# Performance work log

Measured on AMD Instinct MI355X. Metric: run time of the kernel, lower is better.

## Reference

```python
import jax, jax.numpy as jnp
import numpy as np

D_MODEL = 512
D_STATE = 16
D_CONV = 3
EXPAND = 2
D_INNER = EXPAND * D_MODEL          # 1024
DT_RANK = -(-D_MODEL // 16)          # ceil(d_model/16) = 32
BATCH = 2
SEQ = 1024


def setup_inputs() -> dict:
    key = jax.random.key(0)
    ks = jax.random.split(key, 8)
    s = 0.02
    x = jax.random.normal(ks[0], (BATCH, SEQ, D_MODEL), jnp.float32)
    in_proj_w = jax.random.normal(ks[1], (2 * D_INNER, D_MODEL), jnp.float32) * s
    conv_w = jax.random.normal(ks[2], (D_INNER, 1, D_CONV), jnp.float32) * 0.2  # depthwise (out, in/groups=1, K)
    conv_b = jnp.zeros((D_INNER,), jnp.float32)
    x_proj_w = jax.random.normal(ks[3], (DT_RANK + 4 * D_STATE + 1, D_INNER), jnp.float32) * s
    dt_std = DT_RANK ** -0.5
    dt_w = jax.random.uniform(ks[4], (D_INNER, DT_RANK), jnp.float32, -dt_std, dt_std)
    dt = jnp.exp(jax.random.uniform(ks[5], (D_INNER,), jnp.float32)
                 * (np.log(0.1) - np.log(0.001)) + np.log(0.001))
    dt = jnp.maximum(dt, 1e-4)
    dt_b = dt + jnp.log(-jnp.expm1(-dt))  # inverse-softplus init, as in torch code
    A_log = jnp.log(jnp.tile(jnp.arange(1, D_STATE + 1, dtype=jnp.float32)[None, :], (D_INNER, 1)))
    A_imag = np.pi * jax.random.uniform(ks[6], (D_INNER, D_STATE), jnp.float32)
    D_skip = jnp.ones((D_INNER,), jnp.float32)
    out_proj_w = jax.random.normal(ks[7], (D_MODEL, D_INNER), jnp.float32) * s
    return {"x": x, "in_proj_w": in_proj_w, "conv_w": conv_w, "conv_b": conv_b,
            "x_proj_w": x_proj_w, "dt_w": dt_w, "dt_b": dt_b,
            "A_log": A_log, "A_imag": A_imag, "D_skip": D_skip,
            "out_proj_w": out_proj_w}


def _combine(c1, c2):
    # linear recurrence h_t = a_t * h_{t-1} + u_t as an associative op
    a1, u1 = c1
    a2, u2 = c2
    return a1 * a2, a2 * u1 + u2


def reference(x, in_proj_w, conv_w, conv_b, x_proj_w, dt_w, dt_b,
              A_log, A_imag, D_skip, out_proj_w):
    Bsz, L, _ = x.shape
    d_state = A_log.shape[1]
    dt_rank = dt_w.shape[1]

    xz = x @ in_proj_w.T                     # (B, L, 2*D_inner)
    xi, z = jnp.split(xz, 2, axis=-1)

    # causal depthwise conv1d (torch pads both sides K-1 then slices [:L] == left-pad K-1)
    xc = jax.lax.conv_general_dilated(
        xi.transpose(0, 2, 1), conv_w, window_strides=(1,),
        padding=[(D_CONV - 1, 0)], dimension_numbers=("NCH", "OIH", "NCH"),
        feature_group_count=conv_w.shape[0])
    xc = (xc + conv_b[None, :, None]).transpose(0, 2, 1)   # (B, L, D_inner)
    xc = jax.nn.silu(xc)

    A = -jnp.exp(A_log) + 1j * A_imag         # (D_inner, N) complex64

    proj = xc @ x_proj_w.T                     # (B, L, dt_rank + 4N + 1)
    splits = np.cumsum([dt_rank, d_state, d_state, d_state, d_state])
    delta_raw, B_re, B_im, C_re, C_im, lam = jnp.split(proj, splits, axis=-1)
    delta = jax.nn.softplus(delta_raw @ dt_w.T + dt_b)     # (B, L, D_inner)
    lam = jax.nn.sigmoid(lam)                              # (B, L, 1)
    Bc = B_re + 1j * B_im                                  # (B, L, N)
    Cc = C_re + 1j * C_im                                  # (B, L, N)

    # selective_scan_v3 (trapezoidal discretization)
    alpha = jnp.exp(delta[..., None] * A[None, None])      # (B, L, D, N) complex
    Bx = Bc[:, :, None, :] * xc[..., None]                 # (B, L, D, N) complex
    beta = (1.0 - lam)[..., None] * delta[..., None] * alpha
    gamma = lam[..., None] * delta[..., None]
    Bx_prev = jnp.pad(Bx[:, :-1], ((0, 0), (1, 0), (0, 0), (0, 0)))
    u = beta * Bx_prev + gamma * Bx                        # (B, L, D, N) complex

    _, hs = jax.lax.associative_scan(_combine, (alpha, u), axis=1)

    y = jnp.real(jnp.sum(hs * jnp.conj(Cc)[:, :, None, :], axis=-1))  # (B, L, D)
    y = y + D_skip * xc
    out = (y * jax.nn.silu(z)) @ out_proj_w.T              # (B, L, d_model)
    return out
```

## Files before the change

kernel.cpp:

```cpp
#include <hip/hip_runtime.h>

constexpr int B  = 2, L = 1024, DM = 512, DI = 1024, NST = 16, PW = 97;
constexpr int ML = B * L;
constexpr int NCHUNK = 32, CL = L / NCHUNK;
constexpr int NLANES = B * DI * NST;

#define DEV_INLINE __device__ __forceinline__

typedef __attribute__((ext_vector_type(8))) short bf16x8;
typedef __attribute__((ext_vector_type(4))) float f32x4;

DEV_INLINE float sigmoidf_(float x) { return 1.f / (1.f + __expf(-x)); }
DEV_INLINE unsigned short f2bf(float f) {
  unsigned int u = __float_as_uint(f);
  return (unsigned short)((u + 0x7FFFu + ((u >> 16) & 1u)) >> 16);
}

#if __has_builtin(__builtin_amdgcn_exp2f)
#define EXP2F(x) __builtin_amdgcn_exp2f(x)
#else
#define EXP2F(x) exp2f(x)
#endif
#if __has_builtin(__builtin_amdgcn_sinf)
#define SINR(x) __builtin_amdgcn_sinf(x)
#define COSR(x) __builtin_amdgcn_cosf(x)
#else
#define SINR(x) __sinf((x) * 6.2831853f)
#define COSR(x) __cosf((x) * 6.2831853f)
#endif

DEV_INLINE void sincos_poly(float th, float& s, float& c) {
  float t2 = th * th;
  float u = fmaf(t2, -1.9841270e-4f, 8.3333333e-3f);
  u = fmaf(t2, u, -0.16666667f);
  u = fmaf(t2, u, 1.f);
  s = th * u;
  float v = fmaf(t2, -1.3888889e-3f, 4.1666667e-2f);
  v = fmaf(t2, v, -0.5f);
  c = fmaf(t2, v, 1.f);
}

template <int CTRL>
DEV_INLINE float dpp_add(float v) {
  int x = __builtin_amdgcn_update_dpp(0, __float_as_int(v), CTRL, 0xF, 0xF, true);
  return v + __int_as_float(x);
}

__global__ __launch_bounds__(256) void cvt3_k(
    const float* __restrict__ i0, unsigned short* __restrict__ o0, int n0,
    const float* __restrict__ i1, unsigned short* __restrict__ o1, int n1,
    const float* __restrict__ i2, unsigned short* __restrict__ o2, int n2) {
  int i = blockIdx.x * 256 + threadIdx.x;
  const float* in; unsigned short* out; int off;
  if (i < n0)              { in = i0; out = o0; off = i; }
  else if (i < n0 + n1)    { in = i1; out = o1; off = i - n0; }
  else if (i < n0 + n1 + n2) { in = i2; out = o2; off = i - n0 - n1; }
  else return;
  float4 v = ((const float4*)in)[off];
  ((ushort4*)out)[off] = make_ushort4(f2bf(v.x), f2bf(v.y), f2bf(v.z), f2bf(v.w));
}

DEV_INLINE int swz(int row, int kb) { return (row << 7) + (kb ^ ((row & 7) << 4)); }

__global__ __launch_bounds__(256) void gemm_bf16_64(
    const short* __restrict__ A, const short* __restrict__ W,
    float* __restrict__ C, int M, int N, int K) {
  __shared__ char ldsb[16384];
  const int tid = threadIdx.x;
  const int lane = tid & 63, wv = tid >> 6;
  const int bm = blockIdx.y * 64, bn = blockIdx.x * 64;

  f32x4 acc[4];
#pragma unroll
  for (int nb = 0; nb < 4; ++nb) acc[nb] = (f32x4){0.f, 0.f, 0.f, 0.f};

  for (int k0 = 0; k0 < K; k0 += 64) {
#pragma unroll
    for (int i = 0; i < 2; ++i) {
      int off = i * 4096 + tid * 16;
      int row = off >> 7, kb = off & 127;
      bf16x8 va = *(const bf16x8*)(A + (size_t)(bm + row) * K + k0 + (kb >> 1));
      bf16x8 vw = *(const bf16x8*)(W + (size_t)(bn + row) * K + k0 + (kb >> 1));
      *(bf16x8*)(ldsb + swz(row, kb)) = va;
      *(bf16x8*)(ldsb + 8192 + swz(row, kb)) = vw;
    }
    __syncthreads();
#pragma unroll
    for (int ks = 0; ks < 2; ++ks) {
      const int kb = ks * 64 + ((lane >> 4) << 4);
      bf16x8 af = *(const bf16x8*)(ldsb + swz(wv * 16 + (lane & 15), kb));
#pragma unroll
      for (int nb = 0; nb < 4; ++nb) {
        bf16x8 bfv = *(const bf16x8*)(ldsb + 8192 + swz(nb * 16 + (lane & 15), kb));
        acc[nb] = __builtin_amdgcn_mfma_f32_16x16x32_bf16(af, bfv, acc[nb], 0, 0, 0);
      }
    }
    __syncthreads();
  }
#pragma unroll
  for (int nb = 0; nb < 4; ++nb) {
    int col = bn + nb * 16 + (lane & 15);
    int row0 = bm + wv * 16 + ((lane >> 4) << 2);
#pragma unroll
    for (int j = 0; j < 4; ++j)
      C[(size_t)(row0 + j) * N + col] = acc[nb][j];
  }
}

__global__ __launch_bounds__(256) void gemm_bf16_64_sk(
    const short* __restrict__ A, const short* __restrict__ W,
    float* __restrict__ P, int M, int N, int K) {
  __shared__ char ldsb[16384];
  const int tid = threadIdx.x;
  const int lane = tid & 63, wv = tid >> 6;
  const int bm = blockIdx.y * 64, bn = blockIdx.x * 64;
  const int kz = blockIdx.z * 256;
  float* Cp = P + (size_t)blockIdx.z * M * N;

  f32x4 acc[4];
#pragma unroll
  for (int nb = 0; nb < 4; ++nb) acc[nb] = (f32x4){0.f, 0.f, 0.f, 0.f};

  for (int k0 = kz; k0 < kz + 256; k0 += 64) {
#pragma unroll
    for (int i = 0; i < 2; ++i) {
      int off = i * 4096 + tid * 16;
      int row = off >> 7, kb = off & 127;
      bf16x8 va = *(const bf16x8*)(A + (size_t)(bm + row) * K + k0 + (kb >> 1));
      bf16x8 vw = *(const bf16x8*)(W + (size_t)(bn + row) * K + k0 + (kb >> 1));
      *(bf16x8*)(ldsb + swz(row, kb)) = va;
      *(bf16x8*)(ldsb + 8192 + swz(row, kb)) = vw;
    }
    __syncthreads();
#pragma unroll
    for (int ks = 0; ks < 2; ++ks) {
      const int kb = ks * 64 + ((lane >> 4) << 4);
      bf16x8 af = *(const bf16x8*)(ldsb + swz(wv * 16 + (lane & 15), kb));
#pragma unroll
      for (int nb = 0; nb < 4; ++nb) {
        bf16x8 bfv = *(const bf16x8*)(ldsb + 8192 + swz(nb * 16 + (lane & 15), kb));
        acc[nb] = __builtin_amdgcn_mfma_f32_16x16x32_bf16(af, bfv, acc[nb], 0, 0, 0);
      }
    }
    __syncthreads();
  }
#pragma unroll
  for (int nb = 0; nb < 4; ++nb) {
    int col = bn + nb * 16 + (lane & 15);
    int row0 = bm + wv * 16 + ((lane >> 4) << 2);
#pragma unroll
    for (int j = 0; j < 4; ++j)
      Cp[(size_t)(row0 + j) * N + col] = acc[nb][j];
  }
}

__global__ __launch_bounds__(256) void addp4_k(
    const float4* __restrict__ p, float4* __restrict__ out) {
  constexpr int NN = ML * DM / 4;
  int i = blockIdx.x * 256 + threadIdx.x;
  float4 a = p[i], b = p[i + NN], c = p[i + 2 * NN], d = p[i + 3 * NN];
  out[i] = make_float4(a.x + b.x + c.x + d.x, a.y + b.y + c.y + d.y,
                       a.z + b.z + c.z + d.z, a.w + b.w + c.w + d.w);
}

__global__ __launch_bounds__(256) void conv_silu_k(
    const float* __restrict__ xz, const float* __restrict__ cw,
    const float* __restrict__ cb, float* __restrict__ xc, float* __restrict__ sz) {
  int idx = blockIdx.x * 256 + threadIdx.x;
  int m = idx >> 8, d4 = (idx & 255) * 4;
  int t = m & (L - 1);
  const float* base = xz + (size_t)m * (2 * DI);
  float4 r2 = *(const float4*)(base + d4);
  float4 r1 = (t >= 1) ? *(const float4*)(base - 2 * DI + d4) : make_float4(0, 0, 0, 0);
  float4 r0 = (t >= 2) ? *(const float4*)(base - 4 * DI + d4) : make_float4(0, 0, 0, 0);
  float4 zv = *(const float4*)(base + DI + d4);
  float wv[12];
  *(float4*)(wv + 0) = *(const float4*)(cw + d4 * 3 + 0);
  *(float4*)(wv + 4) = *(const float4*)(cw + d4 * 3 + 4);
  *(float4*)(wv + 8) = *(const float4*)(cw + d4 * 3 + 8);
  float4 bv = *(const float4*)(cb + d4);
  float rin0[4] = {r0.x, r0.y, r0.z, r0.w};
  float rin1[4] = {r1.x, r1.y, r1.z, r1.w};
  float rin2[4] = {r2.x, r2.y, r2.z, r2.w};
  float bb[4] = {bv.x, bv.y, bv.z, bv.w};
  float zz[4] = {zv.x, zv.y, zv.z, zv.w};
  float xo[4], zo[4];
#pragma unroll
  for (int j = 0; j < 4; ++j) {
    float v = bb[j];
    v = fmaf(rin0[j], wv[3 * j + 0], v);
    v = fmaf(rin1[j], wv[3 * j + 1], v);
    v = fmaf(rin2[j], wv[3 * j + 2], v);
    xo[j] = v * sigmoidf_(v);
    zo[j] = zz[j] * sigmoidf_(zz[j]);
  }
  *(float4*)(xc + (size_t)idx * 4) = make_float4(xo[0], xo[1], xo[2], xo[3]);
  *(float4*)(sz + (size_t)idx * 4) = make_float4(zo[0], zo[1], zo[2], zo[3]);
}

__global__ __launch_bounds__(512) void proj_delta_k(
    const float* __restrict__ xc, const float* __restrict__ xw,
    const float* __restrict__ dtw, const float* __restrict__ dtb,
    float* __restrict__ bc2f, float* __restrict__ cc2f,
    float* __restrict__ lamv, float2* __restrict__ dx2) {
  __shared__ float xs[4][DI];
  __shared__ float pt[3][4][128];
  __shared__ float dts[4][32];
  const int tid = threadIdx.x;
  const int m0 = blockIdx.x * 4;
  const int nn = tid & 127, qq = tid >> 7;
  for (int i = tid; i < 4 * DI; i += 512)
    xs[i >> 10][i & 1023] = xc[(size_t)m0 * DI + i];
  __syncthreads();
  float s0 = 0.f, s1 = 0.f, s2 = 0.f, s3 = 0.f;
  if (nn < PW) {
    const float* wr = xw + (size_t)nn * DI + qq * 256;
    const int kb = qq * 256;
#pragma unroll 4
    for (int k = 0; k < 256; k += 4) {
      float4 w4 = *(const float4*)(wr + k);
      s0 = fmaf(xs[0][kb + k], w4.x, s0); s0 = fmaf(xs[0][kb + k + 1], w4.y, s0);
      s0 = fmaf(xs[0][kb + k + 2], w4.z, s0); s0 = fmaf(xs[0][kb + k + 3], w4.w, s0);
      s1 = fmaf(xs[1][kb + k], w4.x, s1); s1 = fmaf(xs[1][kb + k + 1], w4.y, s1);
      s1 = fmaf(xs[1][kb + k + 2], w4.z, s1); s1 = fmaf(xs[1][kb + k + 3], w4.w, s1);
      s2 = fmaf(xs[2][kb + k], w4.x, s2); s2 = fmaf(xs[2][kb + k + 1], w4.y, s2);
      s2 = fmaf(xs[2][kb + k + 2], w4.z, s2); s2 = fmaf(xs[2][kb + k + 3], w4.w, s2);
      s3 = fmaf(xs[3][kb + k], w4.x, s3); s3 = fmaf(xs[3][kb + k + 1], w4.y, s3);
      s3 = fmaf(xs[3][kb + k + 2], w4.z, s3); s3 = fmaf(xs[3][kb + k + 3], w4.w, s3);
    }
    if (qq > 0) {
      pt[qq - 1][0][nn] = s0; pt[qq - 1][1][nn] = s1;
      pt[qq - 1][2][nn] = s2; pt[qq - 1][3][nn] = s3;
    }
  }
  __syncthreads();
  if (qq == 0 && nn < PW) {
    s0 += pt[0][0][nn] + pt[1][0][nn] + pt[2][0][nn];
    s1 += pt[0][1][nn] + pt[1][1][nn] + pt[2][1][nn];
    s2 += pt[0][2][nn] + pt[1][2][nn] + pt[2][2][nn];
    s3 += pt[0][3][nn] + pt[1][3][nn] + pt[2][3][nn];
    float sv[4] = {s0, s1, s2, s3};
#pragma unroll
    for (int r = 0; r < 4; ++r) {
      int m = m0 + r;
      float s = sv[r];
      if (nn < 32)        dts[r][nn] = s;
      else if (nn < 48)   bc2f[(m * 16 + nn - 32) * 2 + 0] = s;
      else if (nn < 64)   bc2f[(m * 16 + nn - 48) * 2 + 1] = s;
      else if (nn < 80)   cc2f[(m * 16 + nn - 64) * 2 + 0] = s;
      else if (nn < 96)   cc2f[(m * 16 + nn - 80) * 2 + 1] = s;
      else                lamv[m] = sigmoidf_(s);
    }
  }
  __syncthreads();
  {
    const int d = tid * 2;
    const float4* dtw4 = (const float4*)dtw;
    float2 bb = *(const float2*)(dtb + d);
    float a0[4], a1[4];
#pragma unroll
    for (int r = 0; r < 4; ++r) { a0[r] = bb.x; a1[r] = bb.y; }
#pragma unroll
    for (int kq = 0; kq < 8; ++kq) {
      float4 wa = dtw4[d * 8 + kq];
      float4 wb = dtw4[(d + 1) * 8 + kq];
#pragma unroll
      for (int r = 0; r < 4; ++r) {
        a0[r] = fmaf(dts[r][kq * 4 + 0], wa.x, a0[r]);
        a0[r] = fmaf(dts[r][kq * 4 + 1], wa.y, a0[r]);
        a0[r] = fmaf(dts[r][kq * 4 + 2], wa.z, a0[r]);
        a0[r] = fmaf(dts[r][kq * 4 + 3], wa.w, a0[r]);
        a1[r] = fmaf(dts[r][kq * 4 + 0], wb.x, a1[r]);
        a1[r] = fmaf(dts[r][kq * 4 + 1], wb.y, a1[r]);
        a1[r] = fmaf(dts[r][kq * 4 + 2], wb.z, a1[r]);
        a1[r] = fmaf(dts[r][kq * 4 + 3], wb.w, a1[r]);
      }
    }
#pragma unroll
    for (int r = 0; r < 4; ++r) {
      float x0 = a0[r], x1 = a1[r];
      float dl0 = (x0 > 20.f) ? x0 : log1pf(__expf(x0));
      float dl1 = (x1 > 20.f) ? x1 : log1pf(__expf(x1));
      float4 o = make_float4(dl0, xs[r][d], dl1, xs[r][d + 1]);
      *(float4*)(dx2 + (size_t)(m0 + r) * DI + d) = o;
    }
  }
}

template <bool PASS_B>
__global__ __launch_bounds__(256, 8) void scan_pass(
    const float2* __restrict__ dx2, const float* __restrict__ lamv,
    const float2* __restrict__ bc2, const float2* __restrict__ cc2,
    const float* __restrict__ sz,
    const float* __restrict__ A_log, const float* __restrict__ A_imag,
    const float* __restrict__ D_skip,
    float2* __restrict__ aggA, float2* __restrict__ aggU,
    unsigned short* __restrict__ ybuf) {
  __shared__ float4 qx[CL][17];
  __shared__ float2 bcl[CL][17];
  __shared__ float2 ccl[PASS_B ? CL : 1][17];
  __shared__ float  ylds[PASS_B ? CL : 1][17];

  const int tid = threadIdx.x;
  const int n = tid & 15, ch = tid >> 4;
  const int bx = blockIdx.x, c = blockIdx.y;
  const int b = bx >> 6, d0 = (bx & 63) * 16;
  const int d = d0 + ch;
  const int lane = bx * 256 + tid;
  const int t0 = c * CL, mb = b * L;

  {
    int t = tid >> 3, pr = tid & 7;
    size_t row = (size_t)(mb + t0 + t);
    float4 v = *(const float4*)(dx2 + row * DI + d0 + pr * 2);
    float lamt = lamv[row];
    float g0 = lamt * v.x, g1 = lamt * v.z;
    qx[t][pr * 2 + 0] = make_float4(v.x, v.y, v.x - g0, g0);
    qx[t][pr * 2 + 1] = make_float4(v.z, v.w, v.z - g1, g1);
    float4 bv = *(const float4*)(bc2 + row * 16 + pr * 2);
    bcl[t][pr * 2 + 0] = make_float2(bv.x, bv.y);
    bcl[t][pr * 2 + 1] = make_float2(bv.z, bv.w);
    if constexpr (PASS_B) {
      float4 cv = *(const float4*)(cc2 + row * 16 + pr * 2);
      ccl[t][pr * 2 + 0] = make_float2(cv.x, cv.y);
      ccl[t][pr * 2 + 1] = make_float2(cv.z, cv.w);
    }
  }

  const float Ar = -__expf(A_log[d * 16 + n]);
  const float Arl = Ar * 1.44269504f;
  const float Ai = A_imag[d * 16 + n];

  float Bxpr = 0.f, Bxpi = 0.f;
  if (c > 0) {
    float xp = dx2[(size_t)(mb + t0 - 1) * DI + d].y;
    float2 bp = bc2[(size_t)(mb + t0 - 1) * 16 + n];
    Bxpr = bp.x * xp; Bxpi = bp.y * xp;
  }
  float hr = 0.f, hi = 0.f, S = 0.f, Dsk = 0.f;
  if (PASS_B) {
    if (c > 0) {
      float2 h0 = aggU[(c - 1) * NLANES + lane];
      hr = h0.x; hi = h0.y;
    }
    Dsk = D_skip[d];
  }

  __syncthreads();

#pragma unroll
  for (int t = 0; t < CL; ++t) {
    float4 q = qx[t][ch];
    float2 bv = bcl[t][n];
    float ear = EXP2F(q.x * Arl);
    float sn, cs; sincos_poly(q.x * Ai, sn, cs);
    float ar = ear * cs, ai = ear * sn;
    float Bxr = bv.x * q.y, Bxi = bv.y * q.y;
    float wr = fmaf(q.z, Bxpr, hr), wi = fmaf(q.z, Bxpi, hi);
    hr = fmaf(q.w, Bxr, fmaf(-ai, wi, ar * wr));
    hi = fmaf(q.w, Bxi, fmaf(ai, wr, ar * wi));
    Bxpr = Bxr; Bxpi = Bxi;
    if constexpr (!PASS_B) {
      S += q.x;
    } else {
      float2 cv = ccl[t][n];
      float yc = fmaf(hi, cv.y, hr * cv.x);
      yc = dpp_add<0xB1>(yc);
      yc = dpp_add<0x4E>(yc);
      yc = dpp_add<0x124>(yc);
      yc = dpp_add<0x128>(yc);
      if (n == 0) ylds[t][ch] = fmaf(Dsk, q.y, yc);
    }
  }

  if constexpr (!PASS_B) {
    float earS = EXP2F(S * Arl);
    float rvS = S * Ai * 0.15915494f;
    float AaR = earS * COSR(rvS);
    float AaI = earS * SINR(rvS);
    int idx = c * NLANES + lane;
    aggA[idx] = make_float2(AaR, AaI);
    aggU[idx] = make_float2(hr, hi);
  } else {
    __syncthreads();
    int t = tid >> 3, pr = tid & 7;
    size_t row = (size_t)(mb + t0 + t);
    float2 szv = *(const float2*)(sz + row * DI + d0 + pr * 2);
    float y0 = ylds[t][pr * 2 + 0] * szv.x;
    float y1 = ylds[t][pr * 2 + 1] * szv.y;
    unsigned pk = (unsigned)f2bf(y0) | ((unsigned)f2bf(y1) << 16);
    *(unsigned*)(ybuf + row * DI + d0 + pr * 2) = pk;
  }
}

__global__ __launch_bounds__(256) void scan_combine_k(
    const float2* __restrict__ aggA, float2* __restrict__ aggU) {
  int gid = blockIdx.x * 256 + threadIdx.x;
  float hr = 0.f, hi = 0.f;
#pragma unroll
  for (int c = 0; c < NCHUNK - 1; ++c) {
    float2 a = aggA[c * NLANES + gid];
    float2 u = aggU[c * NLANES + gid];
    float nr = fmaf(a.x, hr, fmaf(-a.y, hi, u.x));
    float ni = fmaf(a.x, hi, fmaf(a.y, hr, u.y));
    hr = nr; hi = ni;
    aggU[c * NLANES + gid] = make_float2(hr, hi);
  }
}

extern "C" void kernel_launch(void* const* d_in, const int* in_sizes, int n_in,
                              void* d_out, int out_size, void* d_ws, size_t ws_size,
                              hipStream_t stream) {
  const float* x        = (const float*)d_in[0];
  const float* in_proj  = (const float*)d_in[1];
  const float* conv_w   = (const float*)d_in[2];
  const float* conv_b   = (const float*)d_in[3];
  const float* x_proj_w = (const float*)d_in[4];
  const float* dt_w     = (const float*)d_in[5];
  const float* dt_b     = (const float*)d_in[6];
  const float* A_log    = (const float*)d_in[7];
  const float* A_imag   = (const float*)d_in[8];
  const float* D_skip   = (const float*)d_in[9];
  const float* out_proj = (const float*)d_in[10];
  float* out = (float*)d_out;

  float* ws = (float*)d_ws;
  float*  xz    = ws; ws += (size_t)ML * 2 * DI;
  float*  xc    = ws; ws += (size_t)ML * DI;
  float*  sz    = ws; ws += (size_t)ML * DI;
  float2* dx2   = (float2*)ws; ws += (size_t)ML * DI * 2;
  float*  bc2f  = ws; ws += (size_t)ML * 32;
  float*  cc2f  = ws; ws += (size_t)ML * 32;
  float*  lamv  = ws; ws += ML;
  float2* aggA  = (float2*)ws; ws += (size_t)NCHUNK * NLANES * 2;
  float2* aggU  = (float2*)ws; ws += (size_t)NCHUNK * NLANES * 2;
  unsigned short* xb   = (unsigned short*)ws; ws += (size_t)ML * DM / 2;
  unsigned short* wb1  = (unsigned short*)ws; ws += (size_t)(2 * DI) * DM / 2;
  unsigned short* wb2  = (unsigned short*)ws; ws += (size_t)DM * DI / 2;
  unsigned short* ybuf = (unsigned short*)ws; ws += (size_t)ML * DI / 2;

  const int n0 = ML * DM / 4, n1 = 2 * DI * DM / 4, n2 = DM * DI / 4;
  cvt3_k<<<(n0 + n1 + n2 + 255) / 256, 256, 0, stream>>>(x, xb, n0, in_proj, wb1, n1,
                                                         out_proj, wb2, n2);
  gemm_bf16_64<<<dim3(2 * DI / 64, ML / 64), 256, 0, stream>>>(
      (const short*)xb, (const short*)wb1, xz, ML, 2 * DI, DM);
  conv_silu_k<<<ML * DI / 4 / 256, 256, 0, stream>>>(xz, conv_w, conv_b, xc, sz);
  proj_delta_k<<<ML / 4, 512, 0, stream>>>(xc, x_proj_w, dt_w, dt_b,
                                           bc2f, cc2f, lamv, dx2);
  scan_pass<false><<<dim3(128, NCHUNK - 1), 256, 0, stream>>>(
      dx2, lamv, (const float2*)bc2f, (const float2*)cc2f, sz,
      A_log, A_imag, D_skip, aggA, aggU, nullptr);
  scan_combine_k<<<NLANES / 256, 256, 0, stream>>>(aggA, aggU);
  scan_pass<true><<<dim3(128, NCHUNK), 256, 0, stream>>>(
      dx2, lamv, (const float2*)bc2f, (const float2*)cc2f, sz,
      A_log, A_imag, D_skip, aggA, aggU, ybuf);
  gemm_bf16_64_sk<<<dim3(DM / 64, ML / 64, 4), 256, 0, stream>>>(
      (const short*)ybuf, (const short*)wb2, xz, ML, DM, DI);
  addp4_k<<<ML * DM / 4 / 256, 256, 0, stream>>>((const float4*)xz, (float4*)out);
}
```

Before: 141.2 us.

## Split x_proj into tiled split-K FP32 GEMM plus reduce and delta kernels

```diff
diff --git a/kernel.cpp b/kernel.cpp
--- a/kernel.cpp
+++ b/kernel.cpp
@@ -60,6 +60,14 @@
   ((ushort4*)out)[off] = make_ushort4(f2bf(v.x), f2bf(v.y), f2bf(v.z), f2bf(v.w));
 }
 
+__global__ __launch_bounds__(256) void padw_k(
+    const float* __restrict__ xw, float* __restrict__ xwp) {
+  int i = blockIdx.x * 256 + threadIdx.x;
+  int row = i >> 8;
+  float4 v = (row < PW) ? ((const float4*)xw)[i] : make_float4(0, 0, 0, 0);
+  ((float4*)xwp)[i] = v;
+}
+
 DEV_INLINE int swz(int row, int kb) { return (row << 7) + (kb ^ ((row & 7) << 4)); }
 
 __global__ __launch_bounds__(256) void gemm_bf16_64(
@@ -161,6 +169,63 @@
   float4 a = p[i], b = p[i + NN], c = p[i + 2 * NN], d = p[i + 3 * NN];
   out[i] = make_float4(a.x + b.x + c.x + d.x, a.y + b.y + c.y + d.y,
                        a.z + b.z + c.z + d.z, a.w + b.w + c.w + d.w);
+}
+
+__global__ __launch_bounds__(256) void proj_sk_f32(
+    const float* __restrict__ A, const float* __restrict__ W,
+    float* __restrict__ P) {
+  __shared__ float As[16][68];
+  __shared__ float Ws[16][68];
+  const int tid = threadIdx.x;
+  const int tx = tid & 15, ty = tid >> 4;
+  const int bm = blockIdx.y * 64, bn = blockIdx.x * 64;
+  const int kz = blockIdx.z * 128;
+  float acc[4][4] = {};
+  for (int k0 = kz; k0 < kz + 128; k0 += 16) {
+    const int r = tid >> 2, c4 = (tid & 3) * 4;
+    float4 av = *(const float4*)(A + (size_t)(bm + r) * DI + k0 + c4);
+    float4 wv = *(const float4*)(W + (size_t)(bn + r) * DI + k0 + c4);
+    As[c4 + 0][r] = av.x; As[c4 + 1][r] = av.y; As[c4 + 2][r] = av.z; As[c4 + 3][r] = av.w;
+    Ws[c4 + 0][r] = wv.x; Ws[c4 + 1][r] = wv.y; Ws[c4 + 2][r] = wv.z; Ws[c4 + 3][r] = wv.w;
+    __syncthreads();
+#pragma unroll
+    for (int kk = 0; kk < 16; ++kk) {
+      float a[4], b[4];
+#pragma unroll
+      for (int i = 0; i < 4; ++i) a[i] = As[kk][ty * 4 + i];
+#pragma unroll
+      for (int j = 0; j < 4; ++j) b[j] = Ws[kk][tx * 4 + j];
+#pragma unroll
+      for (int i = 0; i < 4; ++i)
+#pragma unroll
+        for (int j = 0; j < 4; ++j) acc[i][j] = fmaf(a[i], b[j], acc[i][j]);
+    }
+    __syncthreads();
+  }
+  float* Cp = P + (size_t)blockIdx.z * ML * 128;
+#pragma unroll
+  for (int i = 0; i < 4; ++i) {
+    float4 v = make_float4(acc[i][0], acc[i][1], acc[i][2], acc[i][3]);
+    *(float4*)(Cp + (size_t)(bm + ty * 4 + i) * 128 + bn + tx * 4) = v;
+  }
+}
+
+__global__ __launch_bounds__(256) void reduce_pack_k(
+    const float* __restrict__ P, float* __restrict__ dtp,
+    float* __restrict__ bc2f, float* __restrict__ cc2f,
+    float* __restrict__ lamv) {
+  int i = blockIdx.x * 256 + threadIdx.x;
+  int m = i >> 7, c = i & 127;
+  if (c >= PW) return;
+  float s = 0.f;
+#pragma unroll
+  for (int z = 0; z < 8; ++z) s += P[(size_t)z * ML * 128 + i];
+  if (c < 32)       dtp[m * 32 + c] = s;
+  else if (c < 48)  bc2f[(m * 16 + c - 32) * 2 + 0] = s;
+  else if (c < 64)  bc2f[(m * 16 + c - 48) * 2 + 1] = s;
+  else if (c < 80)  cc2f[(m * 16 + c - 64) * 2 + 0] = s;
+  else if (c < 96)  cc2f[(m * 16 + c - 80) * 2 + 1] = s;
+  else              lamv[m] = sigmoidf_(s);
 }
 
 __global__ __launch_bounds__(256) void conv_silu_k(
@@ -198,92 +263,42 @@
   *(float4*)(sz + (size_t)idx * 4) = make_float4(zo[0], zo[1], zo[2], zo[3]);
 }
 
-__global__ __launch_bounds__(512) void proj_delta_k(
-    const float* __restrict__ xc, const float* __restrict__ xw,
-    const float* __restrict__ dtw, const float* __restrict__ dtb,
-    float* __restrict__ bc2f, float* __restrict__ cc2f,
-    float* __restrict__ lamv, float2* __restrict__ dx2) {
-  __shared__ float xs[4][DI];
-  __shared__ float pt[3][4][128];
-  __shared__ float dts[4][32];
+__global__ __launch_bounds__(256) void delta_k(
+    const float* __restrict__ dtp, const float* __restrict__ dtw,
+    const float* __restrict__ dtb, const float* __restrict__ xc,
+    float2* __restrict__ dx2) {
+  __shared__ float ws[256][33];
+  __shared__ float ps[8][32];
   const int tid = threadIdx.x;
-  const int m0 = blockIdx.x * 4;
-  const int nn = tid & 127, qq = tid >> 7;
-  for (int i = tid; i < 4 * DI; i += 512)
-    xs[i >> 10][i & 1023] = xc[(size_t)m0 * DI + i];
+  const int d0 = blockIdx.x * 256;
+  const int m0 = blockIdx.y * 8;
+#pragma unroll
+  for (int j = 0; j < 8; ++j) {
+    int flat = tid * 4 + j * 1024;
+    int r = flat >> 5, c = flat & 31;
+    float4 v = *(const float4*)(dtw + (size_t)d0 * 32 + flat);
+    ws[r][c] = v.x; ws[r][c + 1] = v.y; ws[r][c + 2] = v.z; ws[r][c + 3] = v.w;
+  }
+  { int i = tid >> 5, r = tid & 31;
+    ps[i][r] = dtp[(size_t)(m0 + i) * 32 + r]; }
   __syncthreads();
-  float s0 = 0.f, s1 = 0.f, s2 = 0.f, s3 = 0.f;
-  if (nn < PW) {
-    const float* wr = xw + (size_t)nn * DI + qq * 256;
-    const int kb = qq * 256;
-#pragma unroll 4
-    for (int k = 0; k < 256; k += 4) {
-      float4 w4 = *(const float4*)(wr + k);
-      s0 = fmaf(xs[0][kb + k], w4.x, s0); s0 = fmaf(xs[0][kb + k + 1], w4.y, s0);
-      s0 = fmaf(xs[0][kb + k + 2], w4.z, s0); s0 = fmaf(xs[0][kb + k + 3], w4.w, s0);
-      s1 = fmaf(xs[1][kb + k], w4.x, s1); s1 = fmaf(xs[1][kb + k + 1], w4.y, s1);
-      s1 = fmaf(xs[1][kb + k + 2], w4.z, s1); s1 = fmaf(xs[1][kb + k + 3], w4.w, s1);
-      s2 = fmaf(xs[2][kb + k], w4.x, s2); s2 = fmaf(xs[2][kb + k + 1], w4.y, s2);
-      s2 = fmaf(xs[2][kb + k + 2], w4.z, s2); s2 = fmaf(xs[2][kb + k + 3], w4.w, s2);
-      s3 = fmaf(xs[3][kb + k], w4.x, s3); s3 = fmaf(xs[3][kb + k + 1], w4.y, s3);
-      s3 = fmaf(xs[3][kb + k + 2], w4.z, s3); s3 = fmaf(xs[3][kb + k + 3], w4.w, s3);
-    }
-    if (qq > 0) {
-      pt[qq - 1][0][nn] = s0; pt[qq - 1][1][nn] = s1;
-      pt[qq - 1][2][nn] = s2; pt[qq - 1][3][nn] = s3;
-    }
-  }
-  __syncthreads();
-  if (qq == 0 && nn < PW) {
-    s0 += pt[0][0][nn] + pt[1][0][nn] + pt[2][0][nn];
-    s1 += pt[0][1][nn] + pt[1][1][nn] + pt[2][1][nn];
-    s2 += pt[0][2][nn] + pt[1][2][nn] + pt[2][2][nn];
-    s3 += pt[0][3][nn] + pt[1][3][nn] + pt[2][3][nn];
-    float sv[4] = {s0, s1, s2, s3};
-#pragma unroll
-    for (int r = 0; r < 4; ++r) {
-      int m = m0 + r;
-      float s = sv[r];
-      if (nn < 32)        dts[r][nn] = s;
-      else if (nn < 48)   bc2f[(m * 16 + nn - 32) * 2 + 0] = s;
-      else if (nn < 64)   bc2f[(m * 16 + nn - 48) * 2 + 1] = s;
-      else if (nn < 80)   cc2f[(m * 16 + nn - 64) * 2 + 0] = s;
-      else if (nn < 96)   cc2f[(m * 16 + nn - 80) * 2 + 1] = s;
-      else                lamv[m] = sigmoidf_(s);
-    }
-  }
-  __syncthreads();
-  {
-    const int d = tid * 2;
-    const float4* dtw4 = (const float4*)dtw;
-    float2 bb = *(const float2*)(dtb + d);
-    float a0[4], a1[4];
-#pragma unroll
-    for (int r = 0; r < 4; ++r) { a0[r] = bb.x; a1[r] = bb.y; }
-#pragma unroll
-    for (int kq = 0; kq < 8; ++kq) {
-      float4 wa = dtw4[d * 8 + kq];
-      float4 wb = dtw4[(d + 1) * 8 + kq];
-#pragma unroll
-      for (int r = 0; r < 4; ++r) {
-        a0[r] = fmaf(dts[r][kq * 4 + 0], wa.x, a0[r]);
-        a0[r] = fmaf(dts[r][kq * 4 + 1], wa.y, a0[r]);
-        a0[r] = fmaf(dts[r][kq * 4 + 2], wa.z, a0[r]);
-        a0[r] = fmaf(dts[r][kq * 4 + 3], wa.w, a0[r]);
-        a1[r] = fmaf(dts[r][kq * 4 + 0], wb.x, a1[r]);
-        a1[r] = fmaf(dts[r][kq * 4 + 1], wb.y, a1[r]);
-        a1[r] = fmaf(dts[r][kq * 4 + 2], wb.z, a1[r]);
-        a1[r] = fmaf(dts[r][kq * 4 + 3], wb.w, a1[r]);
-      }
-    }
-#pragma unroll
-    for (int r = 0; r < 4; ++r) {
-      float x0 = a0[r], x1 = a1[r];
-      float dl0 = (x0 > 20.f) ? x0 : log1pf(__expf(x0));
-      float dl1 = (x1 > 20.f) ? x1 : log1pf(__expf(x1));
-      float4 o = make_float4(dl0, xs[r][d], dl1, xs[r][d + 1]);
-      *(float4*)(dx2 + (size_t)(m0 + r) * DI + d) = o;
-    }
+  float s[8];
+  float bias = dtb[d0 + tid];
+#pragma unroll
+  for (int i = 0; i < 8; ++i) s[i] = bias;
+#pragma unroll
+  for (int r = 0; r < 32; ++r) {
+    float wv = ws[tid][r];
+#pragma unroll
+    for (int i = 0; i < 8; ++i) s[i] = fmaf(ps[i][r], wv, s[i]);
+  }
+#pragma unroll
+  for (int i = 0; i < 8; ++i) {
+    float x = s[i];
+    float dlt = (x > 20.f) ? x : log1pf(__expf(x));
+    int m = m0 + i;
+    float xt = xc[(size_t)m * DI + d0 + tid];
+    dx2[(size_t)m * DI + d0 + tid] = make_float2(dlt, xt);
   }
 }
 
@@ -429,9 +444,11 @@
   float*  xc    = ws; ws += (size_t)ML * DI;
   float*  sz    = ws; ws += (size_t)ML * DI;
   float2* dx2   = (float2*)ws; ws += (size_t)ML * DI * 2;
+  float*  dtp   = ws; ws += (size_t)ML * 32;
   float*  bc2f  = ws; ws += (size_t)ML * 32;
   float*  cc2f  = ws; ws += (size_t)ML * 32;
   float*  lamv  = ws; ws += ML;
+  float*  xwp   = ws; ws += (size_t)128 * DI;
   float2* aggA  = (float2*)ws; ws += (size_t)NCHUNK * NLANES * 2;
   float2* aggU  = (float2*)ws; ws += (size_t)NCHUNK * NLANES * 2;
   unsigned short* xb   = (unsigned short*)ws; ws += (size_t)ML * DM / 2;
@@ -442,11 +459,13 @@
   const int n0 = ML * DM / 4, n1 = 2 * DI * DM / 4, n2 = DM * DI / 4;
   cvt3_k<<<(n0 + n1 + n2 + 255) / 256, 256, 0, stream>>>(x, xb, n0, in_proj, wb1, n1,
                                                          out_proj, wb2, n2);
+  padw_k<<<128, 256, 0, stream>>>(x_proj_w, xwp);
   gemm_bf16_64<<<dim3(2 * DI / 64, ML / 64), 256, 0, stream>>>(
       (const short*)xb, (const short*)wb1, xz, ML, 2 * DI, DM);
   conv_silu_k<<<ML * DI / 4 / 256, 256, 0, stream>>>(xz, conv_w, conv_b, xc, sz);
-  proj_delta_k<<<ML / 4, 512, 0, stream>>>(xc, x_proj_w, dt_w, dt_b,
-                                           bc2f, cc2f, lamv, dx2);
+  proj_sk_f32<<<dim3(2, ML / 64, 8), 256, 0, stream>>>(xc, xwp, xz);
+  reduce_pack_k<<<ML * 128 / 256, 256, 0, stream>>>(xz, dtp, bc2f, cc2f, lamv);
+  delta_k<<<dim3(DI / 256, ML / 8), 256, 0, stream>>>(dtp, dt_w, dt_b, xc, dx2);
   scan_pass<false><<<dim3(128, NCHUNK - 1), 256, 0, stream>>>(
       dx2, lamv, (const float2*)bc2f, (const float2*)cc2f, sz,
       A_log, A_imag, D_skip, aggA, aggU, nullptr);
```

New measurement: 141.2 us. Within noise of the previous version (+0.0%).

## Move x_proj onto bf16 MFMA split-K GEMM and stage tiles with global_load_lds

Applied to the files above, without the earlier changes.

```diff
diff --git a/kernel.cpp b/kernel.cpp
--- a/kernel.cpp
+++ b/kernel.cpp
@@ -29,6 +29,16 @@
 #define COSR(x) __cosf((x) * 6.2831853f)
 #endif
 
+#if __has_builtin(__builtin_amdgcn_global_load_lds)
+#define HAVE_GLDS 1
+#define GLOAD16(g, l)                                                         \
+  __builtin_amdgcn_global_load_lds(                                           \
+      (const __attribute__((address_space(1))) unsigned int*)(g),             \
+      (__attribute__((address_space(3))) unsigned int*)(l), 16, 0, 0)
+#else
+#define HAVE_GLDS 0
+#endif
+
 DEV_INLINE void sincos_poly(float th, float& s, float& c) {
   float t2 = th * th;
   float u = fmaf(t2, -1.9841270e-4f, 8.3333333e-3f);
@@ -60,7 +70,45 @@
   ((ushort4*)out)[off] = make_ushort4(f2bf(v.x), f2bf(v.y), f2bf(v.z), f2bf(v.w));
 }
 
+__global__ __launch_bounds__(256) void padw_bf16_k(
+    const float* __restrict__ xw, unsigned short* __restrict__ xwpb) {
+  int i = blockIdx.x * 256 + threadIdx.x;
+  int row = i >> 8;
+  float4 v = (row < PW) ? ((const float4*)xw)[i] : make_float4(0, 0, 0, 0);
+  ((ushort4*)xwpb)[i] = make_ushort4(f2bf(v.x), f2bf(v.y), f2bf(v.z), f2bf(v.w));
+}
+
 DEV_INLINE int swz(int row, int kb) { return (row << 7) + (kb ^ ((row & 7) << 4)); }
+
+#define GEMM_STAGE(Abase, Wbase)                                              \
+  _Pragma("unroll")                                                           \
+  for (int i = 0; i < 2; ++i) {                                               \
+    int off = i * 4096 + tid * 16;                                            \
+    int row = off >> 7, kb = off & 127;                                       \
+    int kel = (kb ^ ((row & 7) << 4)) >> 1;                                   \
+    stage16(Abase + (size_t)(bm + row) * K + k0 + kel, ldsb + off);           \
+    stage16(Wbase + (size_t)(bn + row) * K + k0 + kel, ldsb + 8192 + off);    \
+  }
+
+DEV_INLINE void stage16(const short* g, char* l) {
+#if HAVE_GLDS
+  GLOAD16(g, l);
+#else
+  *(bf16x8*)l = *(const bf16x8*)g;
+#endif
+}
+
+#define GEMM_MFMA_BODY                                                        \
+  _Pragma("unroll")                                                           \
+  for (int ks = 0; ks < 2; ++ks) {                                            \
+    const int kb = ks * 64 + ((lane >> 4) << 4);                              \
+    bf16x8 af = *(const bf16x8*)(ldsb + swz(wv * 16 + (lane & 15), kb));      \
+    _Pragma("unroll")                                                         \
+    for (int nb = 0; nb < 4; ++nb) {                                          \
+      bf16x8 bfv = *(const bf16x8*)(ldsb + 8192 + swz(nb * 16 + (lane & 15), kb)); \
+      acc[nb] = __builtin_amdgcn_mfma_f32_16x16x32_bf16(af, bfv, acc[nb], 0, 0, 0); \
+    }                                                                         \
+  }
 
 __global__ __launch_bounds__(256) void gemm_bf16_64(
     const short* __restrict__ A, const short* __restrict__ W,
@@ -75,26 +123,9 @@
   for (int nb = 0; nb < 4; ++nb) acc[nb] = (f32x4){0.f, 0.f, 0.f, 0.f};
 
   for (int k0 = 0; k0 < K; k0 += 64) {
-#pragma unroll
-    for (int i = 0; i < 2; ++i) {
-      int off = i * 4096 + tid * 16;
-      int row = off >> 7, kb = off & 127;
-      bf16x8 va = *(const bf16x8*)(A + (size_t)(bm + row) * K + k0 + (kb >> 1));
-      bf16x8 vw = *(const bf16x8*)(W + (size_t)(bn + row) * K + k0 + (kb >> 1));
-      *(bf16x8*)(ldsb + swz(row, kb)) = va;
-      *(bf16x8*)(ldsb + 8192 + swz(row, kb)) = vw;
-    }
+    GEMM_STAGE(A, W)
     __syncthreads();
-#pragma unroll
-    for (int ks = 0; ks < 2; ++ks) {
-      const int kb = ks * 64 + ((lane >> 4) << 4);
-      bf16x8 af = *(const bf16x8*)(ldsb + swz(wv * 16 + (lane & 15), kb));
-#pragma unroll
-      for (int nb = 0; nb < 4; ++nb) {
-        bf16x8 bfv = *(const bf16x8*)(ldsb + 8192 + swz(nb * 16 + (lane & 15), kb));
-        acc[nb] = __builtin_amdgcn_mfma_f32_16x16x32_bf16(af, bfv, acc[nb], 0, 0, 0);
-      }
-    }
+    GEMM_MFMA_BODY
     __syncthreads();
   }
 #pragma unroll
@@ -107,41 +138,24 @@
   }
 }
 
-__global__ __launch_bounds__(256) void gemm_bf16_64_sk(
+__global__ __launch_bounds__(256) void gemm_bf16_sk(
     const short* __restrict__ A, const short* __restrict__ W,
-    float* __restrict__ P, int M, int N, int K) {
+    float* __restrict__ P, int M, int N, int K, int KS) {
   __shared__ char ldsb[16384];
   const int tid = threadIdx.x;
   const int lane = tid & 63, wv = tid >> 6;
   const int bm = blockIdx.y * 64, bn = blockIdx.x * 64;
-  const int kz = blockIdx.z * 256;
+  const int kz = blockIdx.z * KS;
   float* Cp = P + (size_t)blockIdx.z * M * N;
 
   f32x4 acc[4];
 #pragma unroll
   for (int nb = 0; nb < 4; ++nb) acc[nb] = (f32x4){0.f, 0.f, 0.f, 0.f};
 
-  for (int k0 = kz; k0 < kz + 256; k0 += 64) {
-#pragma unroll
-    for (int i = 0; i < 2; ++i) {
-      int off = i * 4096 + tid * 16;
-      int row = off >> 7, kb = off & 127;
-      bf16x8 va = *(const bf16x8*)(A + (size_t)(bm + row) * K + k0 + (kb >> 1));
-      bf16x8 vw = *(const bf16x8*)(W + (size_t)(bn + row) * K + k0 + (kb >> 1));
-      *(bf16x8*)(ldsb + swz(row, kb)) = va;
-      *(bf16x8*)(ldsb + 8192 + swz(row, kb)) = vw;
-    }
+  for (int k0 = kz; k0 < kz + KS; k0 += 64) {
+    GEMM_STAGE(A, W)
     __syncthreads();
-#pragma unroll
-    for (int ks = 0; ks < 2; ++ks) {
-      const int kb = ks * 64 + ((lane >> 4) << 4);
-      bf16x8 af = *(const bf16x8*)(ldsb + swz(wv * 16 + (lane & 15), kb));
-#pragma unroll
-      for (int nb = 0; nb < 4; ++nb) {
-        bf16x8 bfv = *(const bf16x8*)(ldsb + 8192 + swz(nb * 16 + (lane & 15), kb));
-        acc[nb] = __builtin_amdgcn_mfma_f32_16x16x32_bf16(af, bfv, acc[nb], 0, 0, 0);
-      }
-    }
+    GEMM_MFMA_BODY
     __syncthreads();
   }
 #pragma unroll
@@ -165,7 +179,8 @@
 
 __global__ __launch_bounds__(256) void conv_silu_k(
     const float* __restrict__ xz, const float* __restrict__ cw,
-    const float* __restrict__ cb, float* __restrict__ xc, float* __restrict__ sz) {
+    const float* __restrict__ cb, float* __restrict__ xc,
+    unsigned short* __restrict__ xcb, float* __restrict__ sz) {
   int idx = blockIdx.x * 256 + threadIdx.x;
   int m = idx >> 8, d4 = (idx & 255) * 4;
   int t = m & (L - 1);
@@ -195,110 +210,77 @@
     zo[j] = zz[j] * sigmoidf_(zz[j]);
   }
   *(float4*)(xc + (size_t)idx * 4) = make_float4(xo[0], xo[1], xo[2], xo[3]);
+  ((ushort4*)xcb)[idx] = make_ushort4(f2bf(xo[0]), f2bf(xo[1]), f2bf(xo[2]), f2bf(xo[3]));
   *(float4*)(sz + (size_t)idx * 4) = make_float4(zo[0], zo[1], zo[2], zo[3]);
 }
 
-__global__ __launch_bounds__(512) void proj_delta_k(
-    const float* __restrict__ xc, const float* __restrict__ xw,
-    const float* __restrict__ dtw, const float* __restrict__ dtb,
-    float* __restrict__ bc2f, float* __restrict__ cc2f,
-    float* __restrict__ lamv, float2* __restrict__ dx2) {
-  __shared__ float xs[4][DI];
-  __shared__ float pt[3][4][128];
-  __shared__ float dts[4][32];
+__global__ __launch_bounds__(256) void reduce_delta_k(
+    const float* __restrict__ P, const float* __restrict__ dtw,
+    const float* __restrict__ dtb, const float* __restrict__ xc,
+    float* __restrict__ bcc4, float* __restrict__ lamv,
+    float2* __restrict__ dx2) {
+  __shared__ float pp[2][32];
   const int tid = threadIdx.x;
-  const int m0 = blockIdx.x * 4;
-  const int nn = tid & 127, qq = tid >> 7;
-  for (int i = tid; i < 4 * DI; i += 512)
-    xs[i >> 10][i & 1023] = xc[(size_t)m0 * DI + i];
+  const int i = blockIdx.x * 256 + tid;
+  const int m = i >> 7, c = i & 127;
+  float s = 0.f;
+#pragma unroll
+  for (int z = 0; z < 8; ++z) s += P[(size_t)z * ML * 128 + i];
+  if (c < 32)       pp[tid >> 7][c] = s;
+  else if (c < 48)  bcc4[(m * 16 + c - 32) * 4 + 0] = s;
+  else if (c < 64)  bcc4[(m * 16 + c - 48) * 4 + 1] = s;
+  else if (c < 80)  bcc4[(m * 16 + c - 64) * 4 + 2] = s;
+  else if (c < 96)  bcc4[(m * 16 + c - 80) * 4 + 3] = s;
+  else if (c == 96) lamv[m] = sigmoidf_(s);
   __syncthreads();
-  float s0 = 0.f, s1 = 0.f, s2 = 0.f, s3 = 0.f;
-  if (nn < PW) {
-    const float* wr = xw + (size_t)nn * DI + qq * 256;
-    const int kb = qq * 256;
-#pragma unroll 4
-    for (int k = 0; k < 256; k += 4) {
-      float4 w4 = *(const float4*)(wr + k);
-      s0 = fmaf(xs[0][kb + k], w4.x, s0); s0 = fmaf(xs[0][kb + k + 1], w4.y, s0);
-      s0 = fmaf(xs[0][kb + k + 2], w4.z, s0); s0 = fmaf(xs[0][kb + k + 3], w4.w, s0);
-      s1 = fmaf(xs[1][kb + k], w4.x, s1); s1 = fmaf(xs[1][kb + k + 1], w4.y, s1);
-      s1 = fmaf(xs[1][kb + k + 2], w4.z, s1); s1 = fmaf(xs[1][kb + k + 3], w4.w, s1);
-      s2 = fmaf(xs[2][kb + k], w4.x, s2); s2 = fmaf(xs[2][kb + k + 1], w4.y, s2);
-      s2 = fmaf(xs[2][kb + k + 2], w4.z, s2); s2 = fmaf(xs[2][kb + k + 3], w4.w, s2);
-      s3 = fmaf(xs[3][kb + k], w4.x, s3); s3 = fmaf(xs[3][kb + k + 1], w4.y, s3);
-      s3 = fmaf(xs[3][kb + k + 2], w4.z, s3); s3 = fmaf(xs[3][kb + k + 3], w4.w, s3);
-    }
-    if (qq > 0) {
-      pt[qq - 1][0][nn] = s0; pt[qq - 1][1][nn] = s1;
-      pt[qq - 1][2][nn] = s2; pt[qq - 1][3][nn] = s3;
-    }
-  }
-  __syncthreads();
-  if (qq == 0 && nn < PW) {
-    s0 += pt[0][0][nn] + pt[1][0][nn] + pt[2][0][nn];
-    s1 += pt[0][1][nn] + pt[1][1][nn] + pt[2][1][nn];
-    s2 += pt[0][2][nn] + pt[1][2][nn] + pt[2][2][nn];
-    s3 += pt[0][3][nn] + pt[1][3][nn] + pt[2][3][nn];
-    float sv[4] = {s0, s1, s2, s3};
-#pragma unroll
-    for (int r = 0; r < 4; ++r) {
-      int m = m0 + r;
-      float s = sv[r];
-      if (nn < 32)        dts[r][nn] = s;
-      else if (nn < 48)   bc2f[(m * 16 + nn - 32) * 2 + 0] = s;
-      else if (nn < 64)   bc2f[(m * 16 + nn - 48) * 2 + 1] = s;
-      else if (nn < 80)   cc2f[(m * 16 + nn - 64) * 2 + 0] = s;
-      else if (nn < 96)   cc2f[(m * 16 + nn - 80) * 2 + 1] = s;
-      else                lamv[m] = sigmoidf_(s);
-    }
-  }
-  __syncthreads();
-  {
-    const int d = tid * 2;
-    const float4* dtw4 = (const float4*)dtw;
-    float2 bb = *(const float2*)(dtb + d);
-    float a0[4], a1[4];
-#pragma unroll
-    for (int r = 0; r < 4; ++r) { a0[r] = bb.x; a1[r] = bb.y; }
+  const int d0 = tid * 4;
+  const int m0 = blockIdx.x * 2;
+  float4 bb4 = *(const float4*)(dtb + d0);
+  float acc[2][4];
+#pragma unroll
+  for (int r = 0; r < 2; ++r) {
+    acc[r][0] = bb4.x; acc[r][1] = bb4.y; acc[r][2] = bb4.z; acc[r][3] = bb4.w;
+  }
+#pragma unroll
+  for (int j = 0; j < 4; ++j) {
+    const float4* wrow = (const float4*)(dtw + (size_t)(d0 + j) * 32);
 #pragma unroll
     for (int kq = 0; kq < 8; ++kq) {
-      float4 wa = dtw4[d * 8 + kq];
-      float4 wb = dtw4[(d + 1) * 8 + kq];
-#pragma unroll
-      for (int r = 0; r < 4; ++r) {
-        a0[r] = fmaf(dts[r][kq * 4 + 0], wa.x, a0[r]);
-        a0[r] = fmaf(dts[r][kq * 4 + 1], wa.y, a0[r]);
-        a0[r] = fmaf(dts[r][kq * 4 + 2], wa.z, a0[r]);
-        a0[r] = fmaf(dts[r][kq * 4 + 3], wa.w, a0[r]);
-        a1[r] = fmaf(dts[r][kq * 4 + 0], wb.x, a1[r]);
-        a1[r] = fmaf(dts[r][kq * 4 + 1], wb.y, a1[r]);
-        a1[r] = fmaf(dts[r][kq * 4 + 2], wb.z, a1[r]);
-        a1[r] = fmaf(dts[r][kq * 4 + 3], wb.w, a1[r]);
+      float4 w4 = wrow[kq];
+#pragma unroll
+      for (int r = 0; r < 2; ++r) {
+        acc[r][j] = fmaf(pp[r][kq * 4 + 0], w4.x, acc[r][j]);
+        acc[r][j] = fmaf(pp[r][kq * 4 + 1], w4.y, acc[r][j]);
+        acc[r][j] = fmaf(pp[r][kq * 4 + 2], w4.z, acc[r][j]);
+        acc[r][j] = fmaf(pp[r][kq * 4 + 3], w4.w, acc[r][j]);
       }
     }
-#pragma unroll
-    for (int r = 0; r < 4; ++r) {
-      float x0 = a0[r], x1 = a1[r];
-      float dl0 = (x0 > 20.f) ? x0 : log1pf(__expf(x0));
-      float dl1 = (x1 > 20.f) ? x1 : log1pf(__expf(x1));
-      float4 o = make_float4(dl0, xs[r][d], dl1, xs[r][d + 1]);
-      *(float4*)(dx2 + (size_t)(m0 + r) * DI + d) = o;
-    }
+  }
+#pragma unroll
+  for (int r = 0; r < 2; ++r) {
+    float4 xv = *(const float4*)(xc + (size_t)(m0 + r) * DI + d0);
+    float dl[4];
+#pragma unroll
+    for (int j = 0; j < 4; ++j) {
+      float xq = acc[r][j];
+      dl[j] = (xq > 20.f) ? xq : log1pf(__expf(xq));
+    }
+    *(float4*)(dx2 + (size_t)(m0 + r) * DI + d0) = make_float4(dl[0], xv.x, dl[1], xv.y);
+    *(float4*)(dx2 + (size_t)(m0 + r) * DI + d0 + 2) = make_float4(dl[2], xv.z, dl[3], xv.w);
   }
 }
 
 template <bool PASS_B>
 __global__ __launch_bounds__(256, 8) void scan_pass(
     const float2* __restrict__ dx2, const float* __restrict__ lamv,
-    const float2* __restrict__ bc2, const float2* __restrict__ cc2,
-    const float* __restrict__ sz,
+    const float4* __restrict__ bcc4, const float* __restrict__ sz,
     const float* __restrict__ A_log, const float* __restrict__ A_imag,
     const float* __restrict__ D_skip,
     float2* __restrict__ aggA, float2* __restrict__ aggU,
     unsigned short* __restrict__ ybuf) {
   __shared__ float4 qx[CL][17];
-  __shared__ float2 bcl[CL][17];
-  __shared__ float2 ccl[PASS_B ? CL : 1][17];
+  __shared__ float2 bcl[PASS_B ? 1 : CL][17];
+  __shared__ float4 bccl[PASS_B ? CL : 1][17];
   __shared__ float  ylds[PASS_B ? CL : 1][17];
 
   const int tid = threadIdx.x;
@@ -317,13 +299,14 @@
     float g0 = lamt * v.x, g1 = lamt * v.z;
     qx[t][pr * 2 + 0] = make_float4(v.x, v.y, v.x - g0, g0);
     qx[t][pr * 2 + 1] = make_float4(v.z, v.w, v.z - g1, g1);
-    float4 bv = *(const float4*)(bc2 + row * 16 + pr * 2);
-    bcl[t][pr * 2 + 0] = make_float2(bv.x, bv.y);
-    bcl[t][pr * 2 + 1] = make_float2(bv.z, bv.w);
+    float4 b0 = bcc4[row * 16 + pr * 2 + 0];
+    float4 b1 = bcc4[row * 16 + pr * 2 + 1];
     if constexpr (PASS_B) {
-      float4 cv = *(const float4*)(cc2 + row * 16 + pr * 2);
-      ccl[t][pr * 2 + 0] = make_float2(cv.x, cv.y);
-      ccl[t][pr * 2 + 1] = make_float2(cv.z, cv.w);
+      bccl[t][pr * 2 + 0] = b0;
+      bccl[t][pr * 2 + 1] = b1;
+    } else {
+      bcl[t][pr * 2 + 0] = make_float2(b0.x, b0.y);
+      bcl[t][pr * 2 + 1] = make_float2(b1.x, b1.y);
     }
   }
 
@@ -334,7 +317,7 @@
   float Bxpr = 0.f, Bxpi = 0.f;
   if (c > 0) {
     float xp = dx2[(size_t)(mb + t0 - 1) * DI + d].y;
-    float2 bp = bc2[(size_t)(mb + t0 - 1) * 16 + n];
+    float4 bp = bcc4[(size_t)(mb + t0 - 1) * 16 + n];
     Bxpr = bp.x * xp; Bxpi = bp.y * xp;
   }
   float hr = 0.f, hi = 0.f, S = 0.f, Dsk = 0.f;
@@ -351,11 +334,18 @@
 #pragma unroll
   for (int t = 0; t < CL; ++t) {
     float4 q = qx[t][ch];
-    float2 bv = bcl[t][n];
+    float Br_, Bi_, Cr_ = 0.f, Ci_ = 0.f;
+    if constexpr (PASS_B) {
+      float4 p = bccl[t][n];
+      Br_ = p.x; Bi_ = p.y; Cr_ = p.z; Ci_ = p.w;
+    } else {
+      float2 p = bcl[t][n];
+      Br_ = p.x; Bi_ = p.y;
+    }
     float ear = EXP2F(q.x * Arl);
     float sn, cs; sincos_poly(q.x * Ai, sn, cs);
     float ar = ear * cs, ai = ear * sn;
-    float Bxr = bv.x * q.y, Bxi = bv.y * q.y;
+    float Bxr = Br_ * q.y, Bxi = Bi_ * q.y;
     float wr = fmaf(q.z, Bxpr, hr), wi = fmaf(q.z, Bxpi, hi);
     hr = fmaf(q.w, Bxr, fmaf(-ai, wi, ar * wr));
     hi = fmaf(q.w, Bxi, fmaf(ai, wr, ar * wi));
@@ -363,8 +353,7 @@
     if constexpr (!PASS_B) {
       S += q.x;
     } else {
-      float2 cv = ccl[t][n];
-      float yc = fmaf(hi, cv.y, hr * cv.x);
+      float yc = fmaf(hi, Ci_, hr * Cr_);
       yc = dpp_add<0xB1>(yc);
       yc = dpp_add<0x4E>(yc);
       yc = dpp_add<0x124>(yc);
@@ -429,32 +418,36 @@
   float*  xc    = ws; ws += (size_t)ML * DI;
   float*  sz    = ws; ws += (size_t)ML * DI;
   float2* dx2   = (float2*)ws; ws += (size_t)ML * DI * 2;
-  float*  bc2f  = ws; ws += (size_t)ML * 32;
-  float*  cc2f  = ws; ws += (size_t)ML * 32;
+  float*  bcc4  = ws; ws += (size_t)ML * 64;
   float*  lamv  = ws; ws += ML;
   float2* aggA  = (float2*)ws; ws += (size_t)NCHUNK * NLANES * 2;
   float2* aggU  = (float2*)ws; ws += (size_t)NCHUNK * NLANES * 2;
   unsigned short* xb   = (unsigned short*)ws; ws += (size_t)ML * DM / 2;
   unsigned short* wb1  = (unsigned short*)ws; ws += (size_t)(2 * DI) * DM / 2;
   unsigned short* wb2  = (unsigned short*)ws; ws += (size_t)DM * DI / 2;
+  unsigned short* xcb  = (unsigned short*)ws; ws += (size_t)ML * DI / 2;
+  unsigned short* xwpb = (unsigned short*)ws; ws += (size_t)128 * DI / 2;
   unsigned short* ybuf = (unsigned short*)ws; ws += (size_t)ML * DI / 2;
 
   const int n0 = ML * DM / 4, n1 = 2 * DI * DM / 4, n2 = DM * DI / 4;
   cvt3_k<<<(n0 + n1 + n2 + 255) / 256, 256, 0, stream>>>(x, xb, n0, in_proj, wb1, n1,
                                                          out_proj, wb2, n2);
+  padw_bf16_k<<<128, 256, 0, stream>>>(x_proj_w, xwpb);
   gemm_bf16_64<<<dim3(2 * DI / 64, ML / 64), 256, 0, stream>>>(
       (const short*)xb, (const short*)wb1, xz, ML, 2 * DI, DM);
-  conv_silu_k<<<ML * DI / 4 / 256, 256, 0, stream>>>(xz, conv_w, conv_b, xc, sz);
-  proj_delta_k<<<ML / 4, 512, 0, stream>>>(xc, x_proj_w, dt_w, dt_b,
-                                           bc2f, cc2f, lamv, dx2);
+  conv_silu_k<<<ML * DI / 4 / 256, 256, 0, stream>>>(xz, conv_w, conv_b, xc, xcb, sz);
+  gemm_bf16_sk<<<dim3(2, ML / 64, 8), 256, 0, stream>>>(
+      (const short*)xcb, (const short*)xwpb, xz, ML, 128, DI, 128);
+  reduce_delta_k<<<ML * 128 / 256, 256, 0, stream>>>(xz, dt_w, dt_b, xc,
+                                                     bcc4, lamv, dx2);
   scan_pass<false><<<dim3(128, NCHUNK - 1), 256, 0, stream>>>(
-      dx2, lamv, (const float2*)bc2f, (const float2*)cc2f, sz,
-      A_log, A_imag, D_skip, aggA, aggU, nullptr);
+      dx2, lamv, (const float4*)bcc4, sz, A_log, A_imag, D_skip,
+      aggA, aggU, nullptr);
   scan_combine_k<<<NLANES / 256, 256, 0, stream>>>(aggA, aggU);
   scan_pass<true><<<dim3(128, NCHUNK), 256, 0, stream>>>(
-      dx2, lamv, (const float2*)bc2f, (const float2*)cc2f, sz,
-      A_log, A_imag, D_skip, aggA, aggU, ybuf);
-  gemm_bf16_64_sk<<<dim3(DM / 64, ML / 64, 4), 256, 0, stream>>>(
-      (const short*)ybuf, (const short*)wb2, xz, ML, DM, DI);
+      dx2, lamv, (const float4*)bcc4, sz, A_log, A_imag, D_skip,
+      aggA, aggU, ybuf);
+  gemm_bf16_sk<<<dim3(DM / 64, ML / 64, 4), 256, 0, stream>>>(
+      (const short*)ybuf, (const short*)wb2, xz, ML, DM, DI, 256);
   addp4_k<<<ML * DM / 4 / 256, 256, 0, stream>>>((const float4*)xz, (float4*)out);
 }
```

After: 130.2 us. -7.8%, faster.
